# Optimization experiments

Measured on AMD Instinct MI355X. Metric: run time of the kernel, lower is better.

The kernel has to match this reference:

```python
import jax, jax.numpy as jnp
import numpy as np

EPS = 1e-5  # BatchNorm1d eps


def _glorot(key, shape):
    fan_in, fan_out = shape[0], shape[1]
    lim = float(np.sqrt(6.0 / (fan_in + fan_out)))
    return jax.random.uniform(key, shape, jnp.float32, -lim, lim)


def setup_inputs() -> dict:
    key = jax.random.key(0)
    ks = jax.random.split(key, 6)
    N, IN, H, OUT = 50000, 128, 64, 64
    E = 800000
    x = jax.random.normal(ks[0], (N, IN), jnp.float32)
    edge_index = jax.random.randint(ks[1], (2, E), 0, N, jnp.int64)
    return {
        "x": x,
        "edge_index": edge_index,
        "W1": _glorot(ks[2], (IN, H)),
        "b1": jnp.zeros((H,), jnp.float32),
        "gamma1": jnp.ones((H,), jnp.float32),
        "beta1": jnp.zeros((H,), jnp.float32),
        "W2": _glorot(ks[3], (H, OUT)),
        "b2": jnp.zeros((OUT,), jnp.float32),
        "gamma2": jnp.ones((OUT,), jnp.float32),
        "beta2": jnp.zeros((OUT,), jnp.float32),
    }


def _gcn_conv(x, W, b, src, dst, norm, n):
    # x' = D^{-1/2} (A + I) D^{-1/2} X W + b  (PyG GCNConv, edge_weight=None)
    h = x @ W                              # [N, F]
    msg = h[src] * norm[:, None]           # gather + scale, [E+N, F]
    out = jax.ops.segment_sum(msg, dst, num_segments=n)  # scatter-add
    return out + b


def _batch_norm(h, gamma, beta):
    # training-mode BN over node dim, biased variance (as torch uses for normalization)
    mean = h.mean(0)
    var = h.var(0)
    return (h - mean) * jax.lax.rsqrt(var + EPS) * gamma + beta


def reference(x, edge_index, W1, b1, gamma1, beta1, W2, b2, gamma2, beta2):
    n = x.shape[0]
    # add self loops
    loop = jnp.arange(n, dtype=edge_index.dtype)
    src = jnp.concatenate([edge_index[0], loop])
    dst = jnp.concatenate([edge_index[1], loop])
    # symmetric degree normalization (deg >= 1 thanks to self loops)
    deg = jax.ops.segment_sum(jnp.ones(src.shape[0], x.dtype), dst, num_segments=n)
    dinv = jax.lax.rsqrt(jnp.maximum(deg, 1e-12))
    norm = dinv[src] * dinv[dst]           # [E+N]

    # layer 1: GCNConv -> BN -> ReLU (dropout = identity in eval)
    h = _gcn_conv(x, W1, b1, src, dst, norm, n)
    h = jax.nn.relu(_batch_norm(h, gamma1, beta1))
    # layer 2: GCNConv -> BN (no activation on last layer)
    h = _gcn_conv(h, W2, b2, src, dst, norm, n)
    h = _batch_norm(h, gamma2, beta2)
    return h
```

## Files before the change

### kernel.cpp

```cpp
#include <hip/hip_runtime.h>
#include <hip/hip_fp16.h>
#include <math.h>

#define EPS 1e-5f
#define CAP 64

typedef float v4f __attribute__((ext_vector_type(4)));

__device__ __forceinline__ float xor32sum(float a) {
    return a + __shfl_xor(a, 32, 64);
}

__global__ void k_init(int* __restrict__ cnt, float* __restrict__ stats,
                       __half* __restrict__ Ylo, __half* __restrict__ Yhi,
                       unsigned short* __restrict__ csr, int N) {
    int i = blockIdx.x * blockDim.x + threadIdx.x;
    if (i < N) {
        cnt[i] = 0;
        int4* p = (int4*)(csr + (size_t)i * CAP);
#pragma unroll
        for (int k = 0; k < 8; ++k) p[k] = make_int4(-1, -1, -1, -1);
    }
    if (i < 256) stats[i] = 0.0f;
    if (i < 16) {
        ((int*)(Ylo + (size_t)N * 32))[i] = 0;
        ((int*)(Yhi + (size_t)N * 32))[i] = 0;
    }
}

__global__ void k_dinv(const int* __restrict__ cnt, float* __restrict__ dinv, int N) {
    int i = blockIdx.x * blockDim.x + threadIdx.x;
    if (i < N) dinv[i] = rsqrtf((float)(cnt[i] + 1));
    if (i == 0) dinv[N] = 0.0f;
}

__global__ __launch_bounds__(256) void k_gemm1_fill(const float* __restrict__ x,
                                                    const float* __restrict__ W1,
                                                    __half* __restrict__ Ylo,
                                                    __half* __restrict__ Yhi, int N,
                                                    const int* __restrict__ src,
                                                    const int* __restrict__ dst,
                                                    int* __restrict__ cnt,
                                                    unsigned short* __restrict__ csr,
                                                    int E, int G) {
    if ((int)blockIdx.x >= G) {
        int t = (blockIdx.x - G) * 256 + threadIdx.x;
        int stride = (gridDim.x - G) * 256;
        for (int e = t; e < E; e += stride) {
            int d = dst[e];
            int pos = atomicAdd(&cnt[d], 1);
            if (pos < CAP)
                __builtin_nontemporal_store((unsigned short)src[e], &csr[(size_t)d * CAP + pos]);
        }
        return;
    }
    __shared__ float w[128 * 64];
    __shared__ float xs[4][4][128];
    for (int i = threadIdx.x; i < 128 * 64; i += 256) w[i] = W1[i];
    __syncthreads();
    int lane = threadIdx.x & 63;
    int wave = threadIdx.x >> 6;
    int half = lane >> 5, l = lane & 31;
    __half* Yout = half ? Yhi : Ylo;
    int gwave = blockIdx.x * 4 + wave;
    int nw = G * 4;
    for (int r0 = gwave * 4; r0 < N; r0 += nw * 4) {
        int nr = min(4, N - r0);
        for (int j = 0; j < nr; ++j) {
            xs[wave][j][lane]      = x[(size_t)(r0 + j) * 128 + lane];
            xs[wave][j][64 + lane] = x[(size_t)(r0 + j) * 128 + 64 + lane];
        }
        float a0 = 0.f, a1 = 0.f, a2 = 0.f, a3 = 0.f;
#pragma unroll 8
        for (int k = 0; k < 128; ++k) {
            float wk = w[k * 64 + lane];
            a0 += xs[wave][0][k] * wk;
            a1 += xs[wave][1][k] * wk;
            a2 += xs[wave][2][k] * wk;
            a3 += xs[wave][3][k] * wk;
        }
        Yout[(size_t)(r0 + 0) * 32 + l] = __float2half(a0);
        if (nr > 1) Yout[(size_t)(r0 + 1) * 32 + l] = __float2half(a1);
        if (nr > 2) Yout[(size_t)(r0 + 2) * 32 + l] = __float2half(a2);
        if (nr > 3) Yout[(size_t)(r0 + 3) * 32 + l] = __float2half(a3);
    }
}

template <bool PRESCALED>
__global__ __launch_bounds__(256) void k_agg(const __half* __restrict__ Ylo,
                                             const __half* __restrict__ Yhi,
                                             const unsigned short* __restrict__ csr,
                                             const int* __restrict__ cnt,
                                             const float* __restrict__ dinv,
                                             float* __restrict__ H,
                                             float* __restrict__ stats, int N) {
    __shared__ float ssum[4][32], ssq[4][32];
    int half = blockIdx.x & 1;
    const __half* Y = half ? Yhi : Ylo;
    int lane = threadIdx.x & 63;
    int wave = threadIdx.x >> 6;
    int fl = lane & 7;
    int node = (lane >> 3) & 3;
    int gsh = (lane >> 5) << 4;
    float selfmask = (lane < 32) ? 1.f : 0.f;
    int slot = (blockIdx.x >> 1) * 4 + wave;
    int nslots = (gridDim.x >> 1) * 4;
    float s0 = 0.f, s1 = 0.f, s2 = 0.f, s3 = 0.f;
    float q0 = 0.f, q1 = 0.f, q2 = 0.f, q3 = 0.f;
    union U8 { double d; __half2 h[2]; };
    for (int base = slot * 4; base < N; base += nslots * 4) {
        int myv = base + node;
        bool vok = myv < N;
        int vs = vok ? myv : N;
        int c  = vok ? min(cnt[myv], CAP) : 0;
        float dv = dinv[vs];
        const unsigned int* crow =
            (const unsigned int*)(csr + (size_t)(vok ? myv : 0) * CAP);
        float a0, a1, a2, a3;
        {
            U8 u; u.d = *(const double*)(Y + (size_t)vs * 32 + fl * 4);
            float2 p0 = __half22float2(u.h[0]);
            float2 p1 = __half22float2(u.h[1]);
            float selfw = selfmask * (PRESCALED ? 1.f : dv);
            a0 = selfw * p0.x; a1 = selfw * p0.y;
            a2 = selfw * p1.x; a3 = selfw * p1.y;
        }
        for (int b = 0; b < 32; ++b) {
            if (__all(2 * b >= c)) break;
            unsigned int w = crow[b];
            int ent = vok ? (int)((w >> gsh) & 0xFFFFu) : 0xFFFF;
            int idx = min(ent, N);
            float de = PRESCALED ? 1.f : dinv[idx];
            U8 u; u.d = *(const double*)(Y + (size_t)idx * 32 + fl * 4);
            float2 p0 = __half22float2(u.h[0]);
            float2 p1 = __half22float2(u.h[1]);
            a0 += de * p0.x; a1 += de * p0.y;
            a2 += de * p1.x; a3 += de * p1.y;
        }
        a0 = xor32sum(a0) * dv;
        a1 = xor32sum(a1) * dv;
        a2 = xor32sum(a2) * dv;
        a3 = xor32sum(a3) * dv;
        if (lane < 32 && vok) {
            v4f hv = {a0, a1, a2, a3};
            __builtin_nontemporal_store(hv, (v4f*)(H + (size_t)myv * 64 + half * 32 + fl * 4));
        }
        s0 += a0; s1 += a1; s2 += a2; s3 += a3;
        q0 += a0 * a0; q1 += a1 * a1; q2 += a2 * a2; q3 += a3 * a3;
    }
#pragma unroll
    for (int m = 8; m <= 16; m <<= 1) {
        s0 += __shfl_xor(s0, m, 64); s1 += __shfl_xor(s1, m, 64);
        s2 += __shfl_xor(s2, m, 64); s3 += __shfl_xor(s3, m, 64);
        q0 += __shfl_xor(q0, m, 64); q1 += __shfl_xor(q1, m, 64);
        q2 += __shfl_xor(q2, m, 64); q3 += __shfl_xor(q3, m, 64);
    }
    if (lane < 8) {
        ssum[wave][4 * fl + 0] = s0; ssum[wave][4 * fl + 1] = s1;
        ssum[wave][4 * fl + 2] = s2; ssum[wave][4 * fl + 3] = s3;
        ssq[wave][4 * fl + 0] = q0;  ssq[wave][4 * fl + 1] = q1;
        ssq[wave][4 * fl + 2] = q2;  ssq[wave][4 * fl + 3] = q3;
    }
    __syncthreads();
    if (threadIdx.x < 32) {
        float ts = ssum[0][threadIdx.x] + ssum[1][threadIdx.x] + ssum[2][threadIdx.x] + ssum[3][threadIdx.x];
        float tq = ssq[0][threadIdx.x] + ssq[1][threadIdx.x] + ssq[2][threadIdx.x] + ssq[3][threadIdx.x];
        atomicAdd(&stats[half * 32 + threadIdx.x], ts);
        atomicAdd(&stats[64 + half * 32 + threadIdx.x], tq);
    }
}

__global__ __launch_bounds__(256) void k_gemm2(const float* __restrict__ H1,
                                               const float* __restrict__ stats,
                                               const float* __restrict__ gamma,
                                               const float* __restrict__ beta,
                                               const float* __restrict__ W2,
                                               const float* __restrict__ dinv,
                                               __half* __restrict__ Ylo,
                                               __half* __restrict__ Yhi, int N) {
    __shared__ float w[64 * 64];
    __shared__ float xs[4][4][64];
    for (int i = threadIdx.x; i < 64 * 64; i += 256) w[i] = W2[i];
    int lane = threadIdx.x & 63;
    int wave = threadIdx.x >> 6;
    int half = lane >> 5, l = lane & 31;
    __half* Yout = half ? Yhi : Ylo;
    float mean = stats[lane] / (float)N;
    float var = stats[64 + lane] / (float)N - mean * mean;
    float rstd = rsqrtf(var + EPS);
    float g = gamma[lane], bt = beta[lane];
    __syncthreads();
    int gwave = blockIdx.x * 4 + wave;
    int nw = gridDim.x * 4;
    for (int r0 = gwave * 4; r0 < N; r0 += nw * 4) {
        int nr = min(4, N - r0);
        for (int j = 0; j < nr; ++j) {
            float v = H1[(size_t)(r0 + j) * 64 + lane];
            v = (v - mean) * rstd * g + bt;
            xs[wave][j][lane] = fmaxf(v, 0.f);
        }
        float a0 = 0.f, a1 = 0.f, a2 = 0.f, a3 = 0.f;
#pragma unroll 8
        for (int k = 0; k < 64; ++k) {
            float wk = w[k * 64 + lane];
            a0 += xs[wave][0][k] * wk;
            a1 += xs[wave][1][k] * wk;
            a2 += xs[wave][2][k] * wk;
            a3 += xs[wave][3][k] * wk;
        }
        Yout[(size_t)(r0 + 0) * 32 + l] = __float2half(a0 * dinv[r0]);
        if (nr > 1) Yout[(size_t)(r0 + 1) * 32 + l] = __float2half(a1 * dinv[r0 + 1]);
        if (nr > 2) Yout[(size_t)(r0 + 2) * 32 + l] = __float2half(a2 * dinv[r0 + 2]);
        if (nr > 3) Yout[(size_t)(r0 + 3) * 32 + l] = __float2half(a3 * dinv[r0 + 3]);
    }
}

__global__ void k_bnfinal(float* __restrict__ out, const float* __restrict__ stats,
                          const float* __restrict__ gamma, const float* __restrict__ beta,
                          int N) {
    int i = blockIdx.x * blockDim.x + threadIdx.x;
    int total = N * 64;
    if (i < total) {
        int f = i & 63;
        float mean = stats[f] / (float)N;
        float var = stats[64 + f] / (float)N - mean * mean;
        float rstd = rsqrtf(var + EPS);
        out[i] = (out[i] - mean) * rstd * gamma[f] + beta[f];
    }
}

extern "C" void kernel_launch(void* const* d_in, const int* in_sizes, int n_in,
                              void* d_out, int out_size, void* d_ws, size_t ws_size,
                              hipStream_t stream) {
    const float* x      = (const float*)d_in[0];
    const int*   ei     = (const int*)d_in[1];
    const float* W1     = (const float*)d_in[2];
    const float* gamma1 = (const float*)d_in[4];
    const float* beta1  = (const float*)d_in[5];
    const float* W2     = (const float*)d_in[6];
    const float* gamma2 = (const float*)d_in[8];
    const float* beta2  = (const float*)d_in[9];
    float* out = (float*)d_out;

    const int N = in_sizes[0] / 128;
    const int E = in_sizes[1] / 2;
    const int* src = ei;
    const int* dst = ei + E;

    char* ws = (char*)d_ws;
    int*   cnt   = (int*)  ws;
    float* stats = (float*)(ws + 0x40000);
    float* dinv  = (float*)(ws + 0x50000);
    __half* Ylo  = (__half*)(ws + 0x90000);
    __half* Yhi  = (__half*)(ws + 0x90000 + 0x320000);
    float* H1    = (float*)(ws + 0x90000 + 0x640000);
    unsigned short* csr = (unsigned short*)(ws + 0x90000 + 0x640000 + 0xC40000);

    const int B = (N + 255) / 256;
    const int total = N * 64;
    const int G = 768, F = 256;

    k_init<<<B, 256, 0, stream>>>(cnt, stats, Ylo, Yhi, csr, N);

    k_gemm1_fill<<<G + F, 256, 0, stream>>>(x, W1, Ylo, Yhi, N, src, dst, cnt, csr, E, G);
    k_dinv<<<B, 256, 0, stream>>>(cnt, dinv, N);
    k_agg<false><<<1250, 256, 0, stream>>>(Ylo, Yhi, csr, cnt, dinv, H1, stats, N);

    k_gemm2<<<1024, 256, 0, stream>>>(H1, stats, gamma1, beta1, W2, dinv, Ylo, Yhi, N);
    k_agg<true><<<1250, 256, 0, stream>>>(Ylo, Yhi, csr, cnt, dinv, out, stats + 128, N);
    k_bnfinal<<<(total + 255) / 256, 256, 0, stream>>>(out, stats + 128, gamma2, beta2, N);
}
```

Before: 265.3 us.

## Prescale layer-1 features by dinv and widen aggregation loads to 16 bytes

Replaces the dinv kernel with a scale kernel that computes dinv and multiplies both fp16 feature halves by it in place. Layer-1 aggregation can then drop the per-neighbor dinv gather and share one kernel with layer 2. The aggregation lane mapping changes so each lane loads 8 halves (16 bytes) and four lane groups process neighbors in parallel. This adds an extra shuffle reduction, doubles the accumulator registers, and adds a rounding step when the prescaled values are stored back to fp16.

```diff
diff --git a/kernel.cpp b/kernel.cpp
--- a/kernel.cpp
+++ b/kernel.cpp
@@ -26,12 +26,6 @@
         ((int*)(Ylo + (size_t)N * 32))[i] = 0;
         ((int*)(Yhi + (size_t)N * 32))[i] = 0;
     }
-}
-
-__global__ void k_dinv(const int* __restrict__ cnt, float* __restrict__ dinv, int N) {
-    int i = blockIdx.x * blockDim.x + threadIdx.x;
-    if (i < N) dinv[i] = rsqrtf((float)(cnt[i] + 1));
-    if (i == 0) dinv[N] = 0.0f;
 }
 
 __global__ __launch_bounds__(256) void k_gemm1_fill(const float* __restrict__ x,
@@ -86,7 +80,29 @@
     }
 }
 
-template <bool PRESCALED>
+__global__ void k_scale(const int* __restrict__ cnt, float* __restrict__ dinv,
+                        __half* __restrict__ Ylo, __half* __restrict__ Yhi, int N) {
+    int i = blockIdx.x * blockDim.x + threadIdx.x;
+    if (i == 0) dinv[N] = 0.0f;
+    int row = i >> 2, c4 = i & 3;
+    if (row >= N) return;
+    float dv = rsqrtf((float)(cnt[row] + 1));
+    if (c4 == 0) dinv[row] = dv;
+    union U16 { uint4 u; __half2 h[4]; } t;
+#pragma unroll
+    for (int buf = 0; buf < 2; ++buf) {
+        __half* Y = buf ? Yhi : Ylo;
+        uint4* p = (uint4*)(Y + (size_t)row * 32 + c4 * 8);
+        t.u = *p;
+#pragma unroll
+        for (int k = 0; k < 4; ++k) {
+            float2 f = __half22float2(t.h[k]);
+            t.h[k] = __float22half2_rn(make_float2(f.x * dv, f.y * dv));
+        }
+        *p = t.u;
+    }
+}
+
 __global__ __launch_bounds__(256) void k_agg(const __half* __restrict__ Ylo,
                                              const __half* __restrict__ Yhi,
                                              const unsigned short* __restrict__ csr,
@@ -99,15 +115,18 @@
     const __half* Y = half ? Yhi : Ylo;
     int lane = threadIdx.x & 63;
     int wave = threadIdx.x >> 6;
-    int fl = lane & 7;
-    int node = (lane >> 3) & 3;
-    int gsh = (lane >> 5) << 4;
-    float selfmask = (lane < 32) ? 1.f : 0.f;
+    int fl = lane & 3;
+    int node = (lane >> 2) & 3;
+    int g = lane >> 4;
+    int gd = g >> 1;
+    int gsh = (g & 1) << 4;
+    float selfmask = (g == 0) ? 1.f : 0.f;
     int slot = (blockIdx.x >> 1) * 4 + wave;
     int nslots = (gridDim.x >> 1) * 4;
-    float s0 = 0.f, s1 = 0.f, s2 = 0.f, s3 = 0.f;
-    float q0 = 0.f, q1 = 0.f, q2 = 0.f, q3 = 0.f;
-    union U8 { double d; __half2 h[2]; };
+    float s[8], q[8];
+#pragma unroll
+    for (int j = 0; j < 8; ++j) { s[j] = 0.f; q[j] = 0.f; }
+    union U16 { uint4 u; __half2 h[4]; };
     for (int base = slot * 4; base < N; base += nslots * 4) {
         int myv = base + node;
         bool vok = myv < N;
@@ -116,50 +135,55 @@
         float dv = dinv[vs];
         const unsigned int* crow =
             (const unsigned int*)(csr + (size_t)(vok ? myv : 0) * CAP);
-        float a0, a1, a2, a3;
+        float a[8];
         {
-            U8 u; u.d = *(const double*)(Y + (size_t)vs * 32 + fl * 4);
-            float2 p0 = __half22float2(u.h[0]);
-            float2 p1 = __half22float2(u.h[1]);
-            float selfw = selfmask * (PRESCALED ? 1.f : dv);
-            a0 = selfw * p0.x; a1 = selfw * p0.y;
-            a2 = selfw * p1.x; a3 = selfw * p1.y;
-        }
-        for (int b = 0; b < 32; ++b) {
-            if (__all(2 * b >= c)) break;
-            unsigned int w = crow[b];
+            U16 t; t.u = *(const uint4*)(Y + (size_t)vs * 32 + fl * 8);
+#pragma unroll
+            for (int k = 0; k < 4; ++k) {
+                float2 f = __half22float2(t.h[k]);
+                a[2 * k]     = selfmask * f.x;
+                a[2 * k + 1] = selfmask * f.y;
+            }
+        }
+        for (int b = 0; b < 16; ++b) {
+            if (__all(4 * b >= c)) break;
+            unsigned int w = crow[2 * b + gd];
             int ent = vok ? (int)((w >> gsh) & 0xFFFFu) : 0xFFFF;
             int idx = min(ent, N);
-            float de = PRESCALED ? 1.f : dinv[idx];
-            U8 u; u.d = *(const double*)(Y + (size_t)idx * 32 + fl * 4);
-            float2 p0 = __half22float2(u.h[0]);
-            float2 p1 = __half22float2(u.h[1]);
-            a0 += de * p0.x; a1 += de * p0.y;
-            a2 += de * p1.x; a3 += de * p1.y;
-        }
-        a0 = xor32sum(a0) * dv;
-        a1 = xor32sum(a1) * dv;
-        a2 = xor32sum(a2) * dv;
-        a3 = xor32sum(a3) * dv;
-        if (lane < 32 && vok) {
-            v4f hv = {a0, a1, a2, a3};
-            __builtin_nontemporal_store(hv, (v4f*)(H + (size_t)myv * 64 + half * 32 + fl * 4));
-        }
-        s0 += a0; s1 += a1; s2 += a2; s3 += a3;
-        q0 += a0 * a0; q1 += a1 * a1; q2 += a2 * a2; q3 += a3 * a3;
-    }
-#pragma unroll
-    for (int m = 8; m <= 16; m <<= 1) {
-        s0 += __shfl_xor(s0, m, 64); s1 += __shfl_xor(s1, m, 64);
-        s2 += __shfl_xor(s2, m, 64); s3 += __shfl_xor(s3, m, 64);
-        q0 += __shfl_xor(q0, m, 64); q1 += __shfl_xor(q1, m, 64);
-        q2 += __shfl_xor(q2, m, 64); q3 += __shfl_xor(q3, m, 64);
-    }
-    if (lane < 8) {
-        ssum[wave][4 * fl + 0] = s0; ssum[wave][4 * fl + 1] = s1;
-        ssum[wave][4 * fl + 2] = s2; ssum[wave][4 * fl + 3] = s3;
-        ssq[wave][4 * fl + 0] = q0;  ssq[wave][4 * fl + 1] = q1;
-        ssq[wave][4 * fl + 2] = q2;  ssq[wave][4 * fl + 3] = q3;
+            U16 t; t.u = *(const uint4*)(Y + (size_t)idx * 32 + fl * 8);
+#pragma unroll
+            for (int k = 0; k < 4; ++k) {
+                float2 f = __half22float2(t.h[k]);
+                a[2 * k]     += f.x;
+                a[2 * k + 1] += f.y;
+            }
+        }
+#pragma unroll
+        for (int j = 0; j < 8; ++j) {
+            a[j] += __shfl_xor(a[j], 16, 64);
+            a[j] = xor32sum(a[j]) * dv;
+        }
+        if (g == 0 && vok) {
+            v4f lo = {a[0], a[1], a[2], a[3]};
+            v4f hi = {a[4], a[5], a[6], a[7]};
+            float* dst = H + (size_t)myv * 64 + half * 32 + fl * 8;
+            __builtin_nontemporal_store(lo, (v4f*)dst);
+            __builtin_nontemporal_store(hi, (v4f*)(dst + 4));
+        }
+#pragma unroll
+        for (int j = 0; j < 8; ++j) { s[j] += a[j]; q[j] += a[j] * a[j]; }
+    }
+#pragma unroll
+    for (int j = 0; j < 8; ++j) {
+        s[j] += __shfl_xor(s[j], 4, 64); s[j] += __shfl_xor(s[j], 8, 64);
+        q[j] += __shfl_xor(q[j], 4, 64); q[j] += __shfl_xor(q[j], 8, 64);
+    }
+    if (lane < 4) {
+#pragma unroll
+        for (int j = 0; j < 8; ++j) {
+            ssum[wave][fl * 8 + j] = s[j];
+            ssq[wave][fl * 8 + j]  = q[j];
+        }
     }
     __syncthreads();
     if (threadIdx.x < 32) {
@@ -263,10 +287,10 @@
     k_init<<<B, 256, 0, stream>>>(cnt, stats, Ylo, Yhi, csr, N);
 
     k_gemm1_fill<<<G + F, 256, 0, stream>>>(x, W1, Ylo, Yhi, N, src, dst, cnt, csr, E, G);
-    k_dinv<<<B, 256, 0, stream>>>(cnt, dinv, N);
-    k_agg<false><<<1250, 256, 0, stream>>>(Ylo, Yhi, csr, cnt, dinv, H1, stats, N);
+    k_scale<<<(N * 4 + 255) / 256, 256, 0, stream>>>(cnt, dinv, Ylo, Yhi, N);
+    k_agg<<<1250, 256, 0, stream>>>(Ylo, Yhi, csr, cnt, dinv, H1, stats, N);
 
     k_gemm2<<<1024, 256, 0, stream>>>(H1, stats, gamma1, beta1, W2, dinv, Ylo, Yhi, N);
-    k_agg<true><<<1250, 256, 0, stream>>>(Ylo, Yhi, csr, cnt, dinv, out, stats + 128, N);
+    k_agg<<<1250, 256, 0, stream>>>(Ylo, Yhi, csr, cnt, dinv, out, stats + 128, N);
     k_bnfinal<<<(total + 255) / 256, 256, 0, stream>>>(out, stats + 128, gamma2, beta2, N);
 }
```

Result: faster. 248.6 us (-6.3%).
